# Performance work log

Measured on AMD Instinct MI355X. Metric: run time of the kernel, lower is better.

## Reference

```python
import jax, jax.numpy as jnp
import numpy as np

NQ = 4        # nqubits
NLAYERS = 2   # nlayers
DIM = 2 ** NQ # statevector size = 16


def _apply_1q(state, U, wire, batched):
    """Apply a single-qubit gate U on `wire` to state [B, 16].
    U is [B,2,2] if batched else [2,2]. Pennylane wire 0 = most significant bit."""
    B = state.shape[0]
    st = state.reshape((B,) + (2,) * NQ)
    ax = wire + 1
    st = jnp.moveaxis(st, ax, -1).reshape(B, DIM // 2, 2)
    if batched:
        st = jnp.einsum('bij,bkj->bki', U, st)
    else:
        st = jnp.einsum('ij,bkj->bki', U, st)
    st = st.reshape((B,) + (2,) * NQ)  # last axis is the wire axis now
    st = jnp.moveaxis(st, -1, ax)
    return st.reshape(B, DIM)


def _apply_cnot(state, c, t):
    """CNOT with control c, target t on state [B, 16]."""
    B = state.shape[0]
    st = state.reshape((B,) + (2,) * NQ)
    cax, tax = c + 1, t + 1
    s0 = jnp.take(st, 0, axis=cax)  # control=0 slice, axis removed
    s1 = jnp.take(st, 1, axis=cax)  # control=1 slice
    s1 = jnp.flip(s1, axis=tax - (1 if tax > cax else 0))  # X on target
    st = jnp.stack([s0, s1], axis=cax)
    return st.reshape(B, DIM)


def _simulate(angles, qnn_weights):
    """Batched 4-qubit circuit: RX(angles) encoding, then NLAYERS of
    [RY(weights) on each wire, CNOT ring]. Returns <Z_i> per wire: [B, 4]."""
    B = angles.shape[0]
    state = jnp.zeros((B, DIM), dtype=jnp.complex64).at[:, 0].set(1.0)

    # RX encoding (per-sample angles)
    c = jnp.cos(angles / 2)
    s = jnp.sin(angles / 2)
    for w in range(NQ):
        row0 = jnp.stack([c[:, w] + 0j, -1j * s[:, w]], axis=-1)
        row1 = jnp.stack([-1j * s[:, w], c[:, w] + 0j], axis=-1)
        U = jnp.stack([row0, row1], axis=-2)  # [B,2,2] complex64
        state = _apply_1q(state, U, w, batched=True)

    # Entangling layers (shared weights)
    cw = jnp.cos(qnn_weights / 2)
    sw = jnp.sin(qnn_weights / 2)
    for layer in range(NLAYERS):
        for w in range(NQ):
            k = w + layer * NQ
            U = jnp.stack([jnp.stack([cw[k], -sw[k]]),
                           jnp.stack([sw[k], cw[k]])]).astype(jnp.complex64)
            state = _apply_1q(state, U, w, batched=False)
        for w in range(NQ):
            state = _apply_cnot(state, w, (w + 1) % NQ)

    # <Z_i> = P(bit_i = 0) - P(bit_i = 1)
    probs = jnp.abs(state) ** 2  # [B, 16] real float32
    pr = probs.reshape((B,) + (2,) * NQ)
    evs = []
    for w in range(NQ):
        axes = tuple(a for a in range(1, NQ + 1) if a != w + 1)
        marg = pr.sum(axis=axes)  # [B, 2]
        evs.append(marg[:, 0] - marg[:, 1])
    return jnp.stack(evs, axis=-1)  # [B, 4]


def setup_inputs() -> dict:
    key = jax.random.key(0)
    ks = jax.random.split(key, 6)
    B = 131072
    x = jax.random.uniform(ks[0], (B, 28, 28), dtype=jnp.float32) * 255.0
    W_red = jax.random.normal(ks[1], (NQ, 28 * 28), dtype=jnp.float32) * 0.03
    b_red = jax.random.normal(ks[2], (NQ,), dtype=jnp.float32) * 0.01
    qnn_weights = jax.random.uniform(ks[3], (NLAYERS * NQ,), dtype=jnp.float32) * np.pi
    W_out = jax.random.normal(ks[4], (10, NQ), dtype=jnp.float32) * 0.3
    b_out = jax.random.normal(ks[5], (10,), dtype=jnp.float32) * 0.01
    return {"x": x, "W_red": W_red, "b_red": b_red,
            "qnn_weights": qnn_weights, "W_out": W_out, "b_out": b_out}


def reference(x, W_red, b_red, qnn_weights, W_out, b_out):
    B = x.shape[0]
    h = x.reshape(B, -1) / 255.0
    h = h @ W_red.T + b_red                 # [B, 4]
    angles = jnp.tanh(h) * jnp.pi           # [B, 4]
    ev = _simulate(angles, qnn_weights)     # [B, 4]
    return ev @ W_out.T + b_out             # [B, 10]
```

## Files before the change

kernel.cpp:

```cpp
#include <hip/hip_runtime.h>
#include <math.h>

#define PI_F 3.14159265358979323846f

__device__ __forceinline__ float dot4(const float4 a, const float4 b) {
    return a.x * b.x + a.y * b.y + a.z * b.z + a.w * b.w;
}

template<int P>
__device__ __forceinline__ void rx_gate(float (&ar)[16], float (&ai)[16], float c, float s) {
#pragma unroll
    for (int m = 0; m < 8; ++m) {
        const int i0 = ((m >> P) << (P + 1)) | (m & ((1 << P) - 1));
        const int i1 = i0 | (1 << P);
        const float a0r = ar[i0], a0i = ai[i0], a1r = ar[i1], a1i = ai[i1];
        ar[i0] = c * a0r + s * a1i;
        ai[i0] = c * a0i - s * a1r;
        ar[i1] = c * a1r + s * a0i;
        ai[i1] = c * a1i - s * a0r;
    }
}

template<int P>
__device__ __forceinline__ void ry_gate(float (&ar)[16], float (&ai)[16], float c, float s) {
#pragma unroll
    for (int m = 0; m < 8; ++m) {
        const int i0 = ((m >> P) << (P + 1)) | (m & ((1 << P) - 1));
        const int i1 = i0 | (1 << P);
        const float a0r = ar[i0], a0i = ai[i0], a1r = ar[i1], a1i = ai[i1];
        ar[i0] = c * a0r - s * a1r;
        ai[i0] = c * a0i - s * a1i;
        ar[i1] = s * a0r + c * a1r;
        ai[i1] = s * a0i + c * a1i;
    }
}

template<int PC, int PT>
__device__ __forceinline__ void cnot_gate(float (&ar)[16], float (&ai)[16]) {
#pragma unroll
    for (int i = 0; i < 16; ++i) {
        if ((i & (1 << PC)) && !(i & (1 << PT))) {
            const int j = i | (1 << PT);
            float tr = ar[i]; ar[i] = ar[j]; ar[j] = tr;
            float ti = ai[i]; ai[i] = ai[j]; ai[j] = ti;
        }
    }
}

__device__ __forceinline__ float pack_reduce4(int lane, float s0, float s1, float s2, float s3) {
    const bool b1 = (lane & 1) != 0;
    const bool b2 = (lane & 2) != 0;
    const float u01 = (b1 ? s1 : s0) + __shfl_xor(b1 ? s0 : s1, 1);
    const float u23 = (b1 ? s3 : s2) + __shfl_xor(b1 ? s2 : s3, 1);
    float v = (b2 ? u23 : u01) + __shfl_xor(b2 ? u01 : u23, 2);
    v += __shfl_xor(v, 4);
    v += __shfl_xor(v, 8);
    v += __shfl_xor(v, 16);
    v += __shfl_xor(v, 32);
    return v;
}

__global__ __launch_bounds__(256, 4)
void hybrid_qnn_kernel(const float* __restrict__ x,
                       const float* __restrict__ W_red,
                       const float* __restrict__ b_red,
                       const float* __restrict__ qw,
                       const float* __restrict__ W_out,
                       const float* __restrict__ b_out,
                       float* __restrict__ out,
                       int B)
{
    __shared__ float h_lds[64][4];
    __shared__ float qc_lds[8];
    __shared__ float qs_lds[8];
    __shared__ float outStage[640];

    const int t = threadIdx.x;
    const int lane = t & 63;
    const int wave = t >> 6;
    const long long blockBase = (long long)blockIdx.x * 64;
    const long long wbase = blockBase + wave * 16;

    if (t < 8) {
        const float a = 0.5f * qw[t];
        qc_lds[t] = cosf(a);
        qs_lds[t] = sinf(a);
    }

    const float inv255 = 1.0f / 255.0f;

    float4 Wl[3][4];
#pragma unroll
    for (int c = 0; c < 3; ++c) {
#pragma unroll
        for (int j = 0; j < 4; ++j) {
            const float4 w = *(const float4*)(W_red + j * 784 + 4 * (lane + 64 * c));
            Wl[c][j] = make_float4(w.x * inv255, w.y * inv255, w.z * inv255, w.w * inv255);
        }
    }
    const float br0 = b_red[0], br1 = b_red[1], br2 = b_red[2], br3 = b_red[3];

    {
        const int s = lane >> 2;
        const int c = lane & 3;
        const long long samp = wbase + s;
        float4 wt[4];
#pragma unroll
        for (int j = 0; j < 4; ++j) {
            const float4 w = *(const float4*)(W_red + j * 784 + 768 + 4 * c);
            wt[j] = make_float4(w.x * inv255, w.y * inv255, w.z * inv255, w.w * inv255);
        }
        float4 xt = make_float4(0.f, 0.f, 0.f, 0.f);
        if (samp < B) xt = *(const float4*)(x + (size_t)samp * 784 + 768 + 4 * c);
        float d0 = dot4(xt, wt[0]);
        float d1 = dot4(xt, wt[1]);
        float d2 = dot4(xt, wt[2]);
        float d3 = dot4(xt, wt[3]);
        d0 += __shfl_xor(d0, 1); d0 += __shfl_xor(d0, 2);
        d1 += __shfl_xor(d1, 1); d1 += __shfl_xor(d1, 2);
        d2 += __shfl_xor(d2, 1); d2 += __shfl_xor(d2, 2);
        d3 += __shfl_xor(d3, 1); d3 += __shfl_xor(d3, 2);
        if (c == 0 && samp < B) {
            const int srow = wave * 16 + s;
            h_lds[srow][0] = d0 + br0;
            h_lds[srow][1] = d1 + br1;
            h_lds[srow][2] = d2 + br2;
            h_lds[srow][3] = d3 + br3;
        }
    }

    if (wbase + 16 <= B) {
        const float* xbase = x + (size_t)wbase * 784;
        float4 c0 = *(const float4*)(xbase + 4 * lane);
        float4 c1 = *(const float4*)(xbase + 4 * (lane + 64));
        float4 c2 = *(const float4*)(xbase + 4 * (lane + 128));
#pragma unroll
        for (int q = 0; q < 16; ++q) {
            const float4 x0 = c0, x1 = c1, x2 = c2;
            if (q < 15) {
                const float* nb = xbase + (size_t)(q + 1) * 784;
                c0 = *(const float4*)(nb + 4 * lane);
                c1 = *(const float4*)(nb + 4 * (lane + 64));
                c2 = *(const float4*)(nb + 4 * (lane + 128));
            }
            const float s0 = dot4(x0, Wl[0][0]) + dot4(x1, Wl[1][0]) + dot4(x2, Wl[2][0]);
            const float s1 = dot4(x0, Wl[0][1]) + dot4(x1, Wl[1][1]) + dot4(x2, Wl[2][1]);
            const float s2 = dot4(x0, Wl[0][2]) + dot4(x1, Wl[1][2]) + dot4(x2, Wl[2][2]);
            const float s3 = dot4(x0, Wl[0][3]) + dot4(x1, Wl[1][3]) + dot4(x2, Wl[2][3]);
            const float v = pack_reduce4(lane, s0, s1, s2, s3);
            if (lane < 4) h_lds[wave * 16 + q][lane] += v;
        }
    } else {
        for (int q = 0; q < 16; ++q) {
            const long long samp = wbase + q;
            if (samp >= B) break;
            const float* xb = x + (size_t)samp * 784;
            const float4 x0 = *(const float4*)(xb + 4 * lane);
            const float4 x1 = *(const float4*)(xb + 4 * (lane + 64));
            const float4 x2 = *(const float4*)(xb + 4 * (lane + 128));
            const float s0 = dot4(x0, Wl[0][0]) + dot4(x1, Wl[1][0]) + dot4(x2, Wl[2][0]);
            const float s1 = dot4(x0, Wl[0][1]) + dot4(x1, Wl[1][1]) + dot4(x2, Wl[2][1]);
            const float s2 = dot4(x0, Wl[0][2]) + dot4(x1, Wl[1][2]) + dot4(x2, Wl[2][2]);
            const float s3 = dot4(x0, Wl[0][3]) + dot4(x1, Wl[1][3]) + dot4(x2, Wl[2][3]);
            const float v = pack_reduce4(lane, s0, s1, s2, s3);
            if (lane < 4) h_lds[wave * 16 + q][lane] += v;
        }
    }
    __syncthreads();

    if (t < 64 && blockBase + t < B) {
        const float ang0 = tanhf(h_lds[t][0]) * PI_F;
        const float ang1 = tanhf(h_lds[t][1]) * PI_F;
        const float ang2 = tanhf(h_lds[t][2]) * PI_F;
        const float ang3 = tanhf(h_lds[t][3]) * PI_F;
        const float c0 = cosf(0.5f * ang0), sn0 = sinf(0.5f * ang0);
        const float c1 = cosf(0.5f * ang1), sn1 = sinf(0.5f * ang1);
        const float c2 = cosf(0.5f * ang2), sn2 = sinf(0.5f * ang2);
        const float c3 = cosf(0.5f * ang3), sn3 = sinf(0.5f * ang3);

        float ar[16], ai[16];
#pragma unroll
        for (int i = 0; i < 16; ++i) { ar[i] = 0.f; ai[i] = 0.f; }
        ar[0] = 1.f;

        rx_gate<3>(ar, ai, c0, sn0);
        rx_gate<2>(ar, ai, c1, sn1);
        rx_gate<1>(ar, ai, c2, sn2);
        rx_gate<0>(ar, ai, c3, sn3);

#pragma unroll
        for (int layer = 0; layer < 2; ++layer) {
            const int k0 = layer * 4;
            ry_gate<3>(ar, ai, qc_lds[k0 + 0], qs_lds[k0 + 0]);
            ry_gate<2>(ar, ai, qc_lds[k0 + 1], qs_lds[k0 + 1]);
            ry_gate<1>(ar, ai, qc_lds[k0 + 2], qs_lds[k0 + 2]);
            ry_gate<0>(ar, ai, qc_lds[k0 + 3], qs_lds[k0 + 3]);
            cnot_gate<3, 2>(ar, ai);
            cnot_gate<2, 1>(ar, ai);
            cnot_gate<1, 0>(ar, ai);
            cnot_gate<0, 3>(ar, ai);
        }

        float pr[16];
#pragma unroll
        for (int i = 0; i < 16; ++i) pr[i] = ar[i] * ar[i] + ai[i] * ai[i];

        float ev[4];
#pragma unroll
        for (int w = 0; w < 4; ++w) {
            const int p = 3 - w;
            float e = 0.f;
#pragma unroll
            for (int i = 0; i < 16; ++i) e += (i & (1 << p)) ? -pr[i] : pr[i];
            ev[w] = e;
        }

#pragma unroll
        for (int n = 0; n < 10; ++n) {
            float o = b_out[n];
#pragma unroll
            for (int j = 0; j < 4; ++j) o += ev[j] * W_out[n * 4 + j];
            outStage[t * 10 + n] = o;
        }
    }
    __syncthreads();

    const long long outBase = (long long)blockIdx.x * 640;
    const long long outTotal = (long long)B * 10;
#pragma unroll
    for (int i = t; i < 640; i += 256) {
        const long long oi = outBase + i;
        if (oi < outTotal) out[oi] = outStage[i];
    }
}

extern "C" void kernel_launch(void* const* d_in, const int* in_sizes, int n_in,
                              void* d_out, int out_size, void* d_ws, size_t ws_size,
                              hipStream_t stream) {
    const float* x      = (const float*)d_in[0];
    const float* W_red  = (const float*)d_in[1];
    const float* b_red  = (const float*)d_in[2];
    const float* qw     = (const float*)d_in[3];
    const float* W_out  = (const float*)d_in[4];
    const float* b_out  = (const float*)d_in[5];
    float* out = (float*)d_out;

    const int B = in_sizes[0] / 784;
    const int grid = (B + 63) / 64;
    hipLaunchKernelGGL(hybrid_qnn_kernel, dim3(grid), dim3(256), 0, stream,
                       x, W_red, b_red, qw, W_out, b_out, out, B);
}
```

Measured before the change: 81.20 us.

## Stage x rows into LDS via async global_load_lds double buffering

Replaces the register-prefetch loop over 16 samples per wave with direct global-to-LDS loads into a two-slot per-wave buffer. Manual vmcnt waits and sched barriers keep one row in flight while the other is consumed. The aim is to overlap the memory-bound x stream with the dot products without holding prefetched data in registers. In exchange it adds 12 KB of LDS per block, which may lower occupancy, plus an extra LDS read per element. The vmcnt counting is fragile if the compiler inserts other vector memory ops.

```diff
diff --git a/kernel.cpp b/kernel.cpp
--- a/kernel.cpp
+++ b/kernel.cpp
@@ -2,6 +2,19 @@
 #include <math.h>
 
 #define PI_F 3.14159265358979323846f
+
+typedef const __attribute__((address_space(1))) void gas_void;
+typedef __attribute__((address_space(3))) void las_void;
+
+__device__ __forceinline__ void gld_lds16(const void* g, void* l) {
+    __builtin_amdgcn_global_load_lds((gas_void*)g, (las_void*)l, 16, 0, 0);
+}
+
+__device__ __forceinline__ void stage_row(const float* row, float4* buf, int lane) {
+    gld_lds16(row + 0 * 256 + lane * 4, buf + 0 * 64);
+    gld_lds16(row + 1 * 256 + lane * 4, buf + 1 * 64);
+    gld_lds16(row + 2 * 256 + lane * 4, buf + 2 * 64);
+}
 
 __device__ __forceinline__ float dot4(const float4 a, const float4 b) {
     return a.x * b.x + a.y * b.y + a.z * b.z + a.w * b.w;
@@ -70,6 +83,7 @@
                        float* __restrict__ out,
                        int B)
 {
+    __shared__ float4 xstage[4][2][192];
     __shared__ float h_lds[64][4];
     __shared__ float qc_lds[8];
     __shared__ float qs_lds[8];
@@ -131,24 +145,44 @@
 
     if (wbase + 16 <= B) {
         const float* xbase = x + (size_t)wbase * 784;
-        float4 c0 = *(const float4*)(xbase + 4 * lane);
-        float4 c1 = *(const float4*)(xbase + 4 * (lane + 64));
-        float4 c2 = *(const float4*)(xbase + 4 * (lane + 128));
-#pragma unroll
-        for (int q = 0; q < 16; ++q) {
-            const float4 x0 = c0, x1 = c1, x2 = c2;
-            if (q < 15) {
-                const float* nb = xbase + (size_t)(q + 1) * 784;
-                c0 = *(const float4*)(nb + 4 * lane);
-                c1 = *(const float4*)(nb + 4 * (lane + 64));
-                c2 = *(const float4*)(nb + 4 * (lane + 128));
+        float4* b0 = &xstage[wave][0][0];
+        float4* b1 = &xstage[wave][1][0];
+        stage_row(xbase, b0, lane);
+        for (int qq = 0; qq < 16; qq += 2) {
+            stage_row(xbase + (size_t)(qq + 1) * 784, b1, lane);
+            asm volatile("s_waitcnt vmcnt(3)" ::: "memory");
+            __builtin_amdgcn_sched_barrier(0);
+            {
+                const float4 x0 = b0[lane];
+                const float4 x1 = b0[64 + lane];
+                const float4 x2 = b0[128 + lane];
+                const float s0 = dot4(x0, Wl[0][0]) + dot4(x1, Wl[1][0]) + dot4(x2, Wl[2][0]);
+                const float s1 = dot4(x0, Wl[0][1]) + dot4(x1, Wl[1][1]) + dot4(x2, Wl[2][1]);
+                const float s2 = dot4(x0, Wl[0][2]) + dot4(x1, Wl[1][2]) + dot4(x2, Wl[2][2]);
+                const float s3 = dot4(x0, Wl[0][3]) + dot4(x1, Wl[1][3]) + dot4(x2, Wl[2][3]);
+                const float v = pack_reduce4(lane, s0, s1, s2, s3);
+                if (lane < 4) h_lds[wave * 16 + qq][lane] += v;
             }
-            const float s0 = dot4(x0, Wl[0][0]) + dot4(x1, Wl[1][0]) + dot4(x2, Wl[2][0]);
-            const float s1 = dot4(x0, Wl[0][1]) + dot4(x1, Wl[1][1]) + dot4(x2, Wl[2][1]);
-            const float s2 = dot4(x0, Wl[0][2]) + dot4(x1, Wl[1][2]) + dot4(x2, Wl[2][2]);
-            const float s3 = dot4(x0, Wl[0][3]) + dot4(x1, Wl[1][3]) + dot4(x2, Wl[2][3]);
-            const float v = pack_reduce4(lane, s0, s1, s2, s3);
-            if (lane < 4) h_lds[wave * 16 + q][lane] += v;
+            __builtin_amdgcn_sched_barrier(0);
+            if (qq + 2 < 16) {
+                stage_row(xbase + (size_t)(qq + 2) * 784, b0, lane);
+                asm volatile("s_waitcnt vmcnt(3)" ::: "memory");
+            } else {
+                asm volatile("s_waitcnt vmcnt(0)" ::: "memory");
+            }
+            __builtin_amdgcn_sched_barrier(0);
+            {
+                const float4 x0 = b1[lane];
+                const float4 x1 = b1[64 + lane];
+                const float4 x2 = b1[128 + lane];
+                const float s0 = dot4(x0, Wl[0][0]) + dot4(x1, Wl[1][0]) + dot4(x2, Wl[2][0]);
+                const float s1 = dot4(x0, Wl[0][1]) + dot4(x1, Wl[1][1]) + dot4(x2, Wl[2][1]);
+                const float s2 = dot4(x0, Wl[0][2]) + dot4(x1, Wl[1][2]) + dot4(x2, Wl[2][2]);
+                const float s3 = dot4(x0, Wl[0][3]) + dot4(x1, Wl[1][3]) + dot4(x2, Wl[2][3]);
+                const float v = pack_reduce4(lane, s0, s1, s2, s3);
+                if (lane < 4) h_lds[wave * 16 + qq + 1][lane] += v;
+            }
+            __builtin_amdgcn_sched_barrier(0);
         }
     } else {
         for (int q = 0; q < 16; ++q) {
```

After: 83.27 us. 2.6% more time.
